# Optimization experiments

Hardware: AMD Instinct MI355X
Metric: run time of the kernel (lower is better)

Reference implementation:

```python
import jax
import jax.numpy as jnp
import numpy as np

EPS = 1e-06


def _topk_mask(scores, k):
    # scores: (T, E); hard top-k mask along last dim
    _, idx = jax.lax.top_k(scores, k)            # (T, k)
    hard = jax.nn.one_hot(idx, scores.shape[-1]).sum(axis=-2)  # (T, E)
    return hard.astype(bool)


def setup_inputs() -> dict:
    key = jax.random.key(0)
    k1, k2, k3 = jax.random.split(key, 3)
    T, D, E = 8192, 4096, 64
    h_td = jax.random.normal(k1, (T, D), dtype=jnp.float32)
    # eqx.nn.Linear weight layout: (out_features, in_features)
    W = jax.random.normal(k2, (E, D), dtype=jnp.float32) * (1.0 / np.sqrt(D))
    bias_e = jax.random.normal(k3, (E,), dtype=jnp.float32)
    return {"h_td": h_td, "W": W, "bias_e": bias_e, "k": 8}


def reference(h_td, W, bias_e, k):
    # Linear(d_model -> E), no bias in proj; external bias_e added after
    logits_te = jnp.einsum("td,ed->te", h_td, W) + bias_e[None, :]  # (T, E)
    # Soft combine weights always from clean logits
    weight_te = jax.nn.softmax(logits_te, axis=-1)
    # Training path: Gumbel noise on the selection scores only
    gkey = jax.random.key(42)
    u = jax.random.uniform(gkey, logits_te.shape, minval=EPS, maxval=1.0 - EPS)
    g = -jnp.log(-jnp.log(u))
    sel_scores = logits_te + g
    mask_te = _topk_mask(sel_scores, k)
    return (mask_te, weight_te, logits_te)
```

## Files before the change

### kernel.cpp

```cpp
#include <hip/hip_runtime.h>
#include <stdint.h>
#include <math.h>

#define T_DIM 8192
#define D_DIM 4096
#define E_DIM 64
#define TE (T_DIM * E_DIM)
#define GAP_MARGIN 2e-3
#define ROWS 32
#define BK 256
#define NCHUNK (D_DIM / BK)
#define FIX_WAVES 16
#define FIX_COLS (D_DIM / FIX_WAVES)

typedef __attribute__((ext_vector_type(8))) short short8_t;
typedef __attribute__((ext_vector_type(4))) float f32x4;

#define BAR() do {                                            \
    asm volatile("s_waitcnt lgkmcnt(0)" ::: "memory");        \
    __builtin_amdgcn_s_barrier();                             \
    asm volatile("" ::: "memory");                            \
  } while (0)

__device__ __align__(16) short Whi_g[E_DIM * D_DIM];
__device__ __align__(16) short Wlo_g[E_DIM * D_DIM];

__device__ __forceinline__ void threefry2x32_k42(uint32_t x0, uint32_t x1,
                                                 uint32_t& o0, uint32_t& o1) {
  const uint32_t ks0 = 0u, ks1 = 42u;
  const uint32_t ks2 = 0x1BD11BDAu ^ ks0 ^ ks1;
  x0 += ks0; x1 += ks1;
#define TF_RND(r) { x0 += x1; x1 = (x1 << (r)) | (x1 >> (32 - (r))); x1 ^= x0; }
  TF_RND(13) TF_RND(15) TF_RND(26) TF_RND(6)   x0 += ks1; x1 += ks2 + 1u;
  TF_RND(17) TF_RND(29) TF_RND(16) TF_RND(24)  x0 += ks2; x1 += ks0 + 2u;
  TF_RND(13) TF_RND(15) TF_RND(26) TF_RND(6)   x0 += ks0; x1 += ks1 + 3u;
  TF_RND(17) TF_RND(29) TF_RND(16) TF_RND(24)  x0 += ks1; x1 += ks2 + 4u;
  TF_RND(13) TF_RND(15) TF_RND(26) TF_RND(6)   x0 += ks2; x1 += ks0 + 5u;
#undef TF_RND
  o0 = x0; o1 = x1;
}

__device__ __forceinline__ uint32_t jax_random_bits32(uint32_t j) {
  uint32_t o0, o1;
  threefry2x32_k42(0u, j, o0, o1);
  return o0 ^ o1;
}

__device__ __forceinline__ void finalize_row_f64(double logit, int e, int t,
                                                 float& mask_out, float& weight_out,
                                                 double& gap_out) {
  double m = logit;
#pragma unroll
  for (int off = 1; off < 64; off <<= 1) {
    const double om = __shfl_xor(m, off, 64);
    m = (om > m) ? om : m;
  }
  const double pe = exp(logit - m);
  double s = pe;
#pragma unroll
  for (int off = 1; off < 64; off <<= 1) s += __shfl_xor(s, off, 64);
  weight_out = (float)(pe / s);

  const int idx = t * 64 + e;
  const uint32_t bits = jax_random_bits32((uint32_t)idx);
  const float f01 = __uint_as_float((bits >> 9) | 0x3f800000u) - 1.0f;
  const float minv = 1e-6f;
  const float maxv = 0.999999f;
  float u = __fadd_rn(__fmul_rn(f01, maxv - minv), minv);
  u = fmaxf(minv, u);
  const double g = -log(-log((double)u));
  const double sel = logit + g;

  float mask = 0.0f;
  double cur = sel;
  double v8 = 0.0, v9 = 0.0;
  for (int it = 0; it < 9; ++it) {
    double v = cur;
    int vi = e;
#pragma unroll
    for (int off = 1; off < 64; off <<= 1) {
      const double ov = __shfl_xor(v, off, 64);
      const int    oi = __shfl_xor(vi, off, 64);
      if (ov > v || (ov == v && oi < vi)) { v = ov; vi = oi; }
    }
    if (it < 8) {
      if (vi == e) { mask = 1.0f; cur = -__builtin_inf(); }
      if (it == 7) v8 = v;
    } else {
      v9 = v;
    }
  }
  mask_out = mask;
  gap_out = v8 - v9;
}

__device__ __forceinline__ uint16_t f2bf(float f) {
  const uint32_t x = __float_as_uint(f);
  return (uint16_t)((x + 0x7FFFu + ((x >> 16) & 1u)) >> 16);
}

__device__ __forceinline__ void split8(const float4 a, const float4 b,
                                       short8_t& hi, short8_t& lo) {
  const float f[8] = {a.x, a.y, a.z, a.w, b.x, b.y, b.z, b.w};
#pragma unroll
  for (int j = 0; j < 8; ++j) {
    const uint16_t hb = f2bf(f[j]);
    const float fh = __uint_as_float((uint32_t)hb << 16);
    const uint16_t lb = f2bf(f[j] - fh);
    hi[j] = (short)hb;
    lo[j] = (short)lb;
  }
}

__global__ __launch_bounds__(256)
void w_split_kernel(const float* __restrict__ W) {
  const int g = blockIdx.x * 256 + threadIdx.x;
#pragma unroll
  for (int r = 0; r < 2; ++r) {
    const int u = g * 2 + r;
    const int e = u >> 9;
    const int k0 = (u & 511) * 8;
    const float* wp = W + (size_t)e * D_DIM + k0;
    const float4 a = *reinterpret_cast<const float4*>(wp);
    const float4 b = *reinterpret_cast<const float4*>(wp + 4);
    short8_t hi, lo;
    split8(a, b, hi, lo);
    const int ks = k0 >> 5, q = (k0 >> 3) & 3;
    const int subE = e >> 4, ee = e & 15;
    const int idx = ks * 2048 + subE * 512 + q * 128 + ee * 8;
    *reinterpret_cast<short8_t*>(Whi_g + idx) = hi;
    *reinterpret_cast<short8_t*>(Wlo_g + idx) = lo;
  }
}

__global__ __launch_bounds__(512, 2)
void router_mfma_kernel(const float* __restrict__ h,
                        const float* __restrict__ bias,
                        float* __restrict__ out,
                        unsigned char* __restrict__ flags) {
  __shared__ __align__(16) short Ahi[2][ROWS * BK];
  __shared__ __align__(16) short Alo[2][ROWS * BK];
  __shared__ float logits_lds[ROWS * 65];

  const int tid  = threadIdx.x;
  const int wave = tid >> 6;
  const int lane = tid & 63;
  const int m    = wave >> 2;
  const int n    = wave & 3;
  const int row0 = blockIdx.x * ROWS;

  const int r  = tid >> 4;
  const int k0 = (tid & 15) * 16;
  const int sW  = (tid & 15) >> 1;
  const int qW  = ((tid & 15) & 1) * 2;
  const int u0A = sW * 128 + qW * 32 + r;
  const int u0B = u0A + 32;
  const int uA  = u0A ^ ((u0A >> 5) & 7);
  const int uB  = u0B ^ ((u0B >> 5) & 7);
  const float* hst = h + (size_t)(row0 + r) * D_DIM + k0;

  const int ar0 = (lane >> 4) * 32 + m * 16 + (lane & 15);

  const int b_off = n * 512 + (lane >> 4) * 128 + (lane & 15) * 8;

  f32x4 acc = {0.0f, 0.0f, 0.0f, 0.0f};

  float4 Ra0, Ra1, Ra2, Ra3, Rb0, Rb1, Rb2, Rb3;
  Ra0 = *reinterpret_cast<const float4*>(hst + 0);
  Ra1 = *reinterpret_cast<const float4*>(hst + 4);
  Ra2 = *reinterpret_cast<const float4*>(hst + 8);
  Ra3 = *reinterpret_cast<const float4*>(hst + 12);
  Rb0 = *reinterpret_cast<const float4*>(hst + BK + 0);
  Rb1 = *reinterpret_cast<const float4*>(hst + BK + 4);
  Rb2 = *reinterpret_cast<const float4*>(hst + BK + 8);
  Rb3 = *reinterpret_cast<const float4*>(hst + BK + 12);

#define KSTEP(S, BH, BL)                                                       \
  {                                                                            \
    const int ur0_ = (S) * 128 + ar0;                                          \
    const int ur_  = ur0_ ^ ((ur0_ >> 5) & 7);                                 \
    const short8_t ah_ = *reinterpret_cast<const short8_t*>(&Ahi[BUF_][ur_ * 8]); \
    const short8_t al_ = *reinterpret_cast<const short8_t*>(&Alo[BUF_][ur_ * 8]); \
    acc = __builtin_amdgcn_mfma_f32_16x16x32_bf16(al_, BH, acc, 0, 0, 0);      \
    acc = __builtin_amdgcn_mfma_f32_16x16x32_bf16(ah_, BL, acc, 0, 0, 0);      \
    acc = __builtin_amdgcn_mfma_f32_16x16x32_bf16(ah_, BH, acc, 0, 0, 0);      \
  }

#define CHUNK_STEP(R0, R1, R2, R3, BUF, CC)                                    \
  {                                                                            \
    const int BUF_ = (BUF);                                                    \
               \
    const size_t bb_ = (size_t)((CC) * 8) * 2048 + b_off;                      \
    const short8_t BH0 = *reinterpret_cast<const short8_t*>(Whi_g + bb_ + 0 * 2048); \
    const short8_t BH1 = *reinterpret_cast<const short8_t*>(Whi_g + bb_ + 1 * 2048); \
    const short8_t BH2 = *reinterpret_cast<const short8_t*>(Whi_g + bb_ + 2 * 2048); \
    const short8_t BH3 = *reinterpret_cast<const short8_t*>(Whi_g + bb_ + 3 * 2048); \
    const short8_t BH4 = *reinterpret_cast<const short8_t*>(Whi_g + bb_ + 4 * 2048); \
    const short8_t BH5 = *reinterpret_cast<const short8_t*>(Whi_g + bb_ + 5 * 2048); \
    const short8_t BH6 = *reinterpret_cast<const short8_t*>(Whi_g + bb_ + 6 * 2048); \
    const short8_t BH7 = *reinterpret_cast<const short8_t*>(Whi_g + bb_ + 7 * 2048); \
    const short8_t BL0 = *reinterpret_cast<const short8_t*>(Wlo_g + bb_ + 0 * 2048); \
    const short8_t BL1 = *reinterpret_cast<const short8_t*>(Wlo_g + bb_ + 1 * 2048); \
    const short8_t BL2 = *reinterpret_cast<const short8_t*>(Wlo_g + bb_ + 2 * 2048); \
    const short8_t BL3 = *reinterpret_cast<const short8_t*>(Wlo_g + bb_ + 3 * 2048); \
    const short8_t BL4 = *reinterpret_cast<const short8_t*>(Wlo_g + bb_ + 4 * 2048); \
    const short8_t BL5 = *reinterpret_cast<const short8_t*>(Wlo_g + bb_ + 5 * 2048); \
    const short8_t BL6 = *reinterpret_cast<const short8_t*>(Wlo_g + bb_ + 6 * 2048); \
    const short8_t BL7 = *reinterpret_cast<const short8_t*>(Wlo_g + bb_ + 7 * 2048); \
          \
    short8_t hi_, lo_;                                                         \
    split8(R0, R1, hi_, lo_);                                                  \
    *reinterpret_cast<short8_t*>(&Ahi[BUF_][uA * 8]) = hi_;                    \
    *reinterpret_cast<short8_t*>(&Alo[BUF_][uA * 8]) = lo_;                    \
    split8(R2, R3, hi_, lo_);                                                  \
    *reinterpret_cast<short8_t*>(&Ahi[BUF_][uB * 8]) = hi_;                    \
    *reinterpret_cast<short8_t*>(&Alo[BUF_][uB * 8]) = lo_;                    \
    BAR();                                                                     \
                \
    if ((CC) + 2 < NCHUNK) {                                                   \
      const float* p_ = hst + ((CC) + 2) * BK;                                 \
      R0 = *reinterpret_cast<const float4*>(p_ + 0);                           \
      R1 = *reinterpret_cast<const float4*>(p_ + 4);                           \
      R2 = *reinterpret_cast<const float4*>(p_ + 8);                           \
      R3 = *reinterpret_cast<const float4*>(p_ + 12);                          \
    }                                                                          \
    KSTEP(0, BH0, BL0) KSTEP(1, BH1, BL1) KSTEP(2, BH2, BL2)                   \
    KSTEP(3, BH3, BL3) KSTEP(4, BH4, BL4) KSTEP(5, BH5, BL5)                   \
    KSTEP(6, BH6, BL6) KSTEP(7, BH7, BL7)                                      \
  }

  for (int c = 0; c < NCHUNK; c += 2) {
    CHUNK_STEP(Ra0, Ra1, Ra2, Ra3, 0, c)
    CHUNK_STEP(Rb0, Rb1, Rb2, Rb3, 1, c + 1)
  }
#undef CHUNK_STEP
#undef KSTEP

  {
    const int q   = lane >> 4;
    const int col = n * 16 + (lane & 15);
#pragma unroll
    for (int reg = 0; reg < 4; ++reg) {
      const int mr = m * 16 + q * 4 + reg;
      logits_lds[mr * 65 + col] = acc[reg];
    }
  }
  __syncthreads();

  const int e = lane;
  const double be = (double)bias[e];
  for (int rr = 0; rr < 4; ++rr) {
    const int rloc = wave * 4 + rr;
    const int t = row0 + rloc;
    const double logit = (double)logits_lds[rloc * 65 + e] + be;

    float mask, weight;
    double gap;
    finalize_row_f64(logit, e, t, mask, weight, gap);

    const int idx = t * 64 + e;
    out[idx]          = mask;
    out[TE + idx]     = weight;
    out[2 * TE + idx] = (float)logit;
    if (e == 0) flags[t] = (gap < GAP_MARGIN) ? 1 : 0;
  }
}

__global__ __launch_bounds__(1024)
void router_fixup_kernel(const float* __restrict__ h,
                         const float* __restrict__ W,
                         const float* __restrict__ bias,
                         const unsigned char* __restrict__ flags,
                         float* __restrict__ out) {
  const int t = blockIdx.x;
  if (flags[t] == 0) return;

  __shared__ float  h_lds[D_DIM];
  __shared__ double red[FIX_WAVES][64];

  const int tid  = threadIdx.x;
  const int wv   = tid >> 6;
  const int lane = tid & 63;

  {
    const float4* hrow4 = reinterpret_cast<const float4*>(h + (size_t)t * D_DIM);
    reinterpret_cast<float4*>(h_lds)[tid] = hrow4[tid];
  }
  __syncthreads();

  const int e = lane;
  const float* wrow = W + (size_t)e * D_DIM + wv * FIX_COLS;
  const float* hseg = h_lds + wv * FIX_COLS;

  double acc0 = 0.0, acc1 = 0.0, acc2 = 0.0, acc3 = 0.0;
#pragma unroll 4
  for (int c = 0; c < FIX_COLS; c += 16) {
    const float4 w0 = *reinterpret_cast<const float4*>(wrow + c);
    const float4 w1 = *reinterpret_cast<const float4*>(wrow + c + 4);
    const float4 w2 = *reinterpret_cast<const float4*>(wrow + c + 8);
    const float4 w3 = *reinterpret_cast<const float4*>(wrow + c + 12);
    acc0 = fma((double)w0.x, (double)hseg[c + 0], acc0);
    acc0 = fma((double)w0.y, (double)hseg[c + 1], acc0);
    acc0 = fma((double)w0.z, (double)hseg[c + 2], acc0);
    acc0 = fma((double)w0.w, (double)hseg[c + 3], acc0);
    acc1 = fma((double)w1.x, (double)hseg[c + 4], acc1);
    acc1 = fma((double)w1.y, (double)hseg[c + 5], acc1);
    acc1 = fma((double)w1.z, (double)hseg[c + 6], acc1);
    acc1 = fma((double)w1.w, (double)hseg[c + 7], acc1);
    acc2 = fma((double)w2.x, (double)hseg[c + 8], acc2);
    acc2 = fma((double)w2.y, (double)hseg[c + 9], acc2);
    acc2 = fma((double)w2.z, (double)hseg[c + 10], acc2);
    acc2 = fma((double)w2.w, (double)hseg[c + 11], acc2);
    acc3 = fma((double)w3.x, (double)hseg[c + 12], acc3);
    acc3 = fma((double)w3.y, (double)hseg[c + 13], acc3);
    acc3 = fma((double)w3.z, (double)hseg[c + 14], acc3);
    acc3 = fma((double)w3.w, (double)hseg[c + 15], acc3);
  }
  red[wv][e] = (acc0 + acc1) + (acc2 + acc3);
  __syncthreads();

  if (wv == 0) {
    double s = red[0][e];
#pragma unroll
    for (int i = 1; i < FIX_WAVES; ++i) s += red[i][e];
    const double logit = s + (double)bias[e];

    float mask, weight;
    double gap;
    finalize_row_f64(logit, e, t, mask, weight, gap);

    const int idx = t * 64 + e;
    out[idx]          = mask;
    out[TE + idx]     = weight;
    out[2 * TE + idx] = (float)logit;
  }
}

extern "C" void kernel_launch(void* const* d_in, const int* in_sizes, int n_in,
                              void* d_out, int out_size, void* d_ws, size_t ws_size,
                              hipStream_t stream) {
  const float* h    = (const float*)d_in[0];
  const float* W    = (const float*)d_in[1];
  const float* bias = (const float*)d_in[2];
  float* out = (float*)d_out;
  unsigned char* flags = (unsigned char*)d_ws;

  w_split_kernel<<<64, 256, 0, stream>>>(W);
  router_mfma_kernel<<<T_DIM / ROWS, 512, 0, stream>>>(h, bias, out, flags);
  router_fixup_kernel<<<T_DIM, 1024, 0, stream>>>(h, W, bias, flags, out);
}
```

Baseline: 305.7 us.

## Restructure MFMA router to 4 waves with 2 M-tiles each, rework fixup reduction

The main kernel moves from 8 waves (2x4 M/N tiling) to 4 waves that each compute two 16-row M tiles. Each wave loads its W fragments from global once and reuses them for both tiles, halving redundant B loads per block. The h staging becomes coalesced float4 loads with a simpler, unswizzled LDS layout, and a second barrier is added per chunk. The fixup kernel now uses 512 threads, with each wave computing 8 experts over the full row via coalesced W reads and a shuffle reduction instead of per-column strided reads. Risks include LDS bank conflicts from dropping the swizzle, lower occupancy from launch_bounds(256,1), and the extra barrier.

```diff
diff --git a/kernel.cpp b/kernel.cpp
--- a/kernel.cpp
+++ b/kernel.cpp
@@ -10,8 +10,6 @@
 #define ROWS 32
 #define BK 256
 #define NCHUNK (D_DIM / BK)
-#define FIX_WAVES 16
-#define FIX_COLS (D_DIM / FIX_WAVES)
 
 typedef __attribute__((ext_vector_type(8))) short short8_t;
 typedef __attribute__((ext_vector_type(4))) float f32x4;
@@ -97,6 +95,14 @@
 __device__ __forceinline__ uint16_t f2bf(float f) {
   const uint32_t x = __float_as_uint(f);
   return (uint16_t)((x + 0x7FFFu + ((x >> 16) & 1u)) >> 16);
+}
+
+__device__ __forceinline__ void split4(const float4 v, ushort4& hi, ushort4& lo) {
+  float fh;
+  hi.x = f2bf(v.x); fh = __uint_as_float((uint32_t)hi.x << 16); lo.x = f2bf(v.x - fh);
+  hi.y = f2bf(v.y); fh = __uint_as_float((uint32_t)hi.y << 16); lo.y = f2bf(v.y - fh);
+  hi.z = f2bf(v.z); fh = __uint_as_float((uint32_t)hi.z << 16); lo.z = f2bf(v.z - fh);
+  hi.w = f2bf(v.w); fh = __uint_as_float((uint32_t)hi.w << 16); lo.w = f2bf(v.w - fh);
 }
 
 __device__ __forceinline__ void split8(const float4 a, const float4 b,
@@ -133,7 +139,7 @@
   }
 }
 
-__global__ __launch_bounds__(512, 2)
+__global__ __launch_bounds__(256, 1)
 void router_mfma_kernel(const float* __restrict__ h,
                         const float* __restrict__ bias,
                         float* __restrict__ out,
@@ -145,51 +151,59 @@
   const int tid  = threadIdx.x;
   const int wave = tid >> 6;
   const int lane = tid & 63;
-  const int m    = wave >> 2;
-  const int n    = wave & 3;
   const int row0 = blockIdx.x * ROWS;
 
-  const int r  = tid >> 4;
-  const int k0 = (tid & 15) * 16;
-  const int sW  = (tid & 15) >> 1;
-  const int qW  = ((tid & 15) & 1) * 2;
-  const int u0A = sW * 128 + qW * 32 + r;
-  const int u0B = u0A + 32;
-  const int uA  = u0A ^ ((u0A >> 5) & 7);
-  const int uB  = u0B ^ ((u0B >> 5) & 7);
-  const float* hst = h + (size_t)(row0 + r) * D_DIM + k0;
-
-  const int ar0 = (lane >> 4) * 32 + m * 16 + (lane & 15);
-
-  const int b_off = n * 512 + (lane >> 4) * 128 + (lane & 15) * 8;
-
-  f32x4 acc = {0.0f, 0.0f, 0.0f, 0.0f};
-
-  float4 Ra0, Ra1, Ra2, Ra3, Rb0, Rb1, Rb2, Rb3;
-  Ra0 = *reinterpret_cast<const float4*>(hst + 0);
-  Ra1 = *reinterpret_cast<const float4*>(hst + 4);
-  Ra2 = *reinterpret_cast<const float4*>(hst + 8);
-  Ra3 = *reinterpret_cast<const float4*>(hst + 12);
-  Rb0 = *reinterpret_cast<const float4*>(hst + BK + 0);
-  Rb1 = *reinterpret_cast<const float4*>(hst + BK + 4);
-  Rb2 = *reinterpret_cast<const float4*>(hst + BK + 8);
-  Rb3 = *reinterpret_cast<const float4*>(hst + BK + 12);
+  const int r = tid >> 3;
+  const int j = tid & 7;
+  const int qW = j >> 1, halfW = j & 1;
+  const float* hst = h + (size_t)(row0 + r) * D_DIM + j * 4;
+  const int wbase = (qW * 32 + r) * 8 + halfW * 4;
+
+  const int arbase = (lane >> 4) * 32 + (lane & 15);
+
+  const int b_off = wave * 512 + (lane >> 4) * 128 + (lane & 15) * 8;
+
+  f32x4 accA = {0.0f, 0.0f, 0.0f, 0.0f};
+  f32x4 accB = {0.0f, 0.0f, 0.0f, 0.0f};
+
+  float4 Ra0, Ra1, Ra2, Ra3, Ra4, Ra5, Ra6, Ra7;
+  float4 Rb0, Rb1, Rb2, Rb3, Rb4, Rb5, Rb6, Rb7;
+#define LOADSET(P0,P1,P2,P3,P4,P5,P6,P7, CC)                                   \
+  { const float* p_ = hst + (CC) * BK;                                         \
+    P0 = *reinterpret_cast<const float4*>(p_ + 0 * 32);                        \
+    P1 = *reinterpret_cast<const float4*>(p_ + 1 * 32);                        \
+    P2 = *reinterpret_cast<const float4*>(p_ + 2 * 32);                        \
+    P3 = *reinterpret_cast<const float4*>(p_ + 3 * 32);                        \
+    P4 = *reinterpret_cast<const float4*>(p_ + 4 * 32);                        \
+    P5 = *reinterpret_cast<const float4*>(p_ + 5 * 32);                        \
+    P6 = *reinterpret_cast<const float4*>(p_ + 6 * 32);                        \
+    P7 = *reinterpret_cast<const float4*>(p_ + 7 * 32); }
+
+  LOADSET(Ra0,Ra1,Ra2,Ra3,Ra4,Ra5,Ra6,Ra7, 0)
+  LOADSET(Rb0,Rb1,Rb2,Rb3,Rb4,Rb5,Rb6,Rb7, 1)
+
+#define SPLITW(S, RV)                                                          \
+  { ushort4 hi_, lo_;                                                          \
+    split4(RV, hi_, lo_);                                                      \
+    *reinterpret_cast<ushort4*>(&Ahi[BUF_][(S) * 1024 + wbase]) = hi_;         \
+    *reinterpret_cast<ushort4*>(&Alo[BUF_][(S) * 1024 + wbase]) = lo_; }
 
 #define KSTEP(S, BH, BL)                                                       \
-  {                                                                            \
-    const int ur0_ = (S) * 128 + ar0;                                          \
-    const int ur_  = ur0_ ^ ((ur0_ >> 5) & 7);                                 \
-    const short8_t ah_ = *reinterpret_cast<const short8_t*>(&Ahi[BUF_][ur_ * 8]); \
-    const short8_t al_ = *reinterpret_cast<const short8_t*>(&Alo[BUF_][ur_ * 8]); \
-    acc = __builtin_amdgcn_mfma_f32_16x16x32_bf16(al_, BH, acc, 0, 0, 0);      \
-    acc = __builtin_amdgcn_mfma_f32_16x16x32_bf16(ah_, BL, acc, 0, 0, 0);      \
-    acc = __builtin_amdgcn_mfma_f32_16x16x32_bf16(ah_, BH, acc, 0, 0, 0);      \
-  }
-
-#define CHUNK_STEP(R0, R1, R2, R3, BUF, CC)                                    \
-  {                                                                            \
-    const int BUF_ = (BUF);                                                    \
-               \
+  { const int u0_ = (S) * 128 + arbase;                                        \
+    const short8_t ah0 = *reinterpret_cast<const short8_t*>(&Ahi[BUF_][u0_ * 8]);        \
+    const short8_t al0 = *reinterpret_cast<const short8_t*>(&Alo[BUF_][u0_ * 8]);        \
+    const short8_t ah1 = *reinterpret_cast<const short8_t*>(&Ahi[BUF_][(u0_ + 16) * 8]); \
+    const short8_t al1 = *reinterpret_cast<const short8_t*>(&Alo[BUF_][(u0_ + 16) * 8]); \
+    accA = __builtin_amdgcn_mfma_f32_16x16x32_bf16(al0, BH, accA, 0, 0, 0);    \
+    accA = __builtin_amdgcn_mfma_f32_16x16x32_bf16(ah0, BL, accA, 0, 0, 0);    \
+    accA = __builtin_amdgcn_mfma_f32_16x16x32_bf16(ah0, BH, accA, 0, 0, 0);    \
+    accB = __builtin_amdgcn_mfma_f32_16x16x32_bf16(al1, BH, accB, 0, 0, 0);    \
+    accB = __builtin_amdgcn_mfma_f32_16x16x32_bf16(ah1, BL, accB, 0, 0, 0);    \
+    accB = __builtin_amdgcn_mfma_f32_16x16x32_bf16(ah1, BH, accB, 0, 0, 0); }
+
+#define CHUNK_STEP(P0,P1,P2,P3,P4,P5,P6,P7, BUF, CC)                           \
+  { const int BUF_ = (BUF);                                                    \
+                   \
     const size_t bb_ = (size_t)((CC) * 8) * 2048 + b_off;                      \
     const short8_t BH0 = *reinterpret_cast<const short8_t*>(Whi_g + bb_ + 0 * 2048); \
     const short8_t BH1 = *reinterpret_cast<const short8_t*>(Whi_g + bb_ + 1 * 2048); \
@@ -207,50 +221,44 @@
     const short8_t BL5 = *reinterpret_cast<const short8_t*>(Wlo_g + bb_ + 5 * 2048); \
     const short8_t BL6 = *reinterpret_cast<const short8_t*>(Wlo_g + bb_ + 6 * 2048); \
     const short8_t BL7 = *reinterpret_cast<const short8_t*>(Wlo_g + bb_ + 7 * 2048); \
-          \
-    short8_t hi_, lo_;                                                         \
-    split8(R0, R1, hi_, lo_);                                                  \
-    *reinterpret_cast<short8_t*>(&Ahi[BUF_][uA * 8]) = hi_;                    \
-    *reinterpret_cast<short8_t*>(&Alo[BUF_][uA * 8]) = lo_;                    \
-    split8(R2, R3, hi_, lo_);                                                  \
-    *reinterpret_cast<short8_t*>(&Ahi[BUF_][uB * 8]) = hi_;                    \
-    *reinterpret_cast<short8_t*>(&Alo[BUF_][uB * 8]) = lo_;                    \
+               \
+    SPLITW(0, P0) SPLITW(1, P1) SPLITW(2, P2) SPLITW(3, P3)                    \
+    SPLITW(4, P4) SPLITW(5, P5) SPLITW(6, P6) SPLITW(7, P7)                    \
     BAR();                                                                     \
                 \
     if ((CC) + 2 < NCHUNK) {                                                   \
-      const float* p_ = hst + ((CC) + 2) * BK;                                 \
-      R0 = *reinterpret_cast<const float4*>(p_ + 0);                           \
-      R1 = *reinterpret_cast<const float4*>(p_ + 4);                           \
-      R2 = *reinterpret_cast<const float4*>(p_ + 8);                           \
-      R3 = *reinterpret_cast<const float4*>(p_ + 12);                          \
+      LOADSET(P0,P1,P2,P3,P4,P5,P6,P7, (CC) + 2)                               \
     }                                                                          \
     KSTEP(0, BH0, BL0) KSTEP(1, BH1, BL1) KSTEP(2, BH2, BL2)                   \
     KSTEP(3, BH3, BL3) KSTEP(4, BH4, BL4) KSTEP(5, BH5, BL5)                   \
     KSTEP(6, BH6, BL6) KSTEP(7, BH7, BL7)                                      \
+    BAR();           \
   }
 
   for (int c = 0; c < NCHUNK; c += 2) {
-    CHUNK_STEP(Ra0, Ra1, Ra2, Ra3, 0, c)
-    CHUNK_STEP(Rb0, Rb1, Rb2, Rb3, 1, c + 1)
+    CHUNK_STEP(Ra0,Ra1,Ra2,Ra3,Ra4,Ra5,Ra6,Ra7, 0, c)
+    CHUNK_STEP(Rb0,Rb1,Rb2,Rb3,Rb4,Rb5,Rb6,Rb7, 1, c + 1)
   }
 #undef CHUNK_STEP
 #undef KSTEP
+#undef SPLITW
+#undef LOADSET
 
   {
     const int q   = lane >> 4;
-    const int col = n * 16 + (lane & 15);
+    const int col = wave * 16 + (lane & 15);
 #pragma unroll
     for (int reg = 0; reg < 4; ++reg) {
-      const int mr = m * 16 + q * 4 + reg;
-      logits_lds[mr * 65 + col] = acc[reg];
+      logits_lds[(q * 4 + reg) * 65 + col]      = accA[reg];
+      logits_lds[(16 + q * 4 + reg) * 65 + col] = accB[reg];
     }
   }
   __syncthreads();
 
   const int e = lane;
   const double be = (double)bias[e];
-  for (int rr = 0; rr < 4; ++rr) {
-    const int rloc = wave * 4 + rr;
+  for (int rr = 0; rr < 8; ++rr) {
+    const int rloc = wave * 8 + rr;
     const int t = row0 + rloc;
     const double logit = (double)logits_lds[rloc * 65 + e] + be;
 
@@ -266,7 +274,7 @@
   }
 }
 
-__global__ __launch_bounds__(1024)
+__global__ __launch_bounds__(512)
 void router_fixup_kernel(const float* __restrict__ h,
                          const float* __restrict__ W,
                          const float* __restrict__ bias,
@@ -276,7 +284,7 @@
   if (flags[t] == 0) return;
 
   __shared__ float  h_lds[D_DIM];
-  __shared__ double red[FIX_WAVES][64];
+  __shared__ double red[64];
 
   const int tid  = threadIdx.x;
   const int wv   = tid >> 6;
@@ -284,47 +292,36 @@
 
   {
     const float4* hrow4 = reinterpret_cast<const float4*>(h + (size_t)t * D_DIM);
-    reinterpret_cast<float4*>(h_lds)[tid] = hrow4[tid];
+    float4* hl4 = reinterpret_cast<float4*>(h_lds);
+    hl4[tid]       = hrow4[tid];
+    hl4[tid + 512] = hrow4[tid + 512];
   }
   __syncthreads();
 
-  const int e = lane;
-  const float* wrow = W + (size_t)e * D_DIM + wv * FIX_COLS;
-  const float* hseg = h_lds + wv * FIX_COLS;
-
-  double acc0 = 0.0, acc1 = 0.0, acc2 = 0.0, acc3 = 0.0;
-#pragma unroll 4
-  for (int c = 0; c < FIX_COLS; c += 16) {
-    const float4 w0 = *reinterpret_cast<const float4*>(wrow + c);
-    const float4 w1 = *reinterpret_cast<const float4*>(wrow + c + 4);
-    const float4 w2 = *reinterpret_cast<const float4*>(wrow + c + 8);
-    const float4 w3 = *reinterpret_cast<const float4*>(wrow + c + 12);
-    acc0 = fma((double)w0.x, (double)hseg[c + 0], acc0);
-    acc0 = fma((double)w0.y, (double)hseg[c + 1], acc0);
-    acc0 = fma((double)w0.z, (double)hseg[c + 2], acc0);
-    acc0 = fma((double)w0.w, (double)hseg[c + 3], acc0);
-    acc1 = fma((double)w1.x, (double)hseg[c + 4], acc1);
-    acc1 = fma((double)w1.y, (double)hseg[c + 5], acc1);
-    acc1 = fma((double)w1.z, (double)hseg[c + 6], acc1);
-    acc1 = fma((double)w1.w, (double)hseg[c + 7], acc1);
-    acc2 = fma((double)w2.x, (double)hseg[c + 8], acc2);
-    acc2 = fma((double)w2.y, (double)hseg[c + 9], acc2);
-    acc2 = fma((double)w2.z, (double)hseg[c + 10], acc2);
-    acc2 = fma((double)w2.w, (double)hseg[c + 11], acc2);
-    acc3 = fma((double)w3.x, (double)hseg[c + 12], acc3);
-    acc3 = fma((double)w3.y, (double)hseg[c + 13], acc3);
-    acc3 = fma((double)w3.z, (double)hseg[c + 14], acc3);
-    acc3 = fma((double)w3.w, (double)hseg[c + 15], acc3);
-  }
-  red[wv][e] = (acc0 + acc1) + (acc2 + acc3);
+  for (int ei = 0; ei < 8; ++ei) {
+    const int e = wv * 8 + ei;
+    const float4* wrow = reinterpret_cast<const float4*>(W + (size_t)e * D_DIM);
+    const float4* hl4  = reinterpret_cast<const float4*>(h_lds);
+    double a0 = 0.0, a1 = 0.0, a2 = 0.0, a3 = 0.0;
+#pragma unroll
+    for (int i = 0; i < 16; ++i) {
+      const float4 w  = wrow[i * 64 + lane];
+      const float4 hh = hl4[i * 64 + lane];
+      a0 = fma((double)w.x, (double)hh.x, a0);
+      a1 = fma((double)w.y, (double)hh.y, a1);
+      a2 = fma((double)w.z, (double)hh.z, a2);
+      a3 = fma((double)w.w, (double)hh.w, a3);
+    }
+    double s = (a0 + a1) + (a2 + a3);
+#pragma unroll
+    for (int off = 1; off < 64; off <<= 1) s += __shfl_xor(s, off, 64);
+    if (lane == 0) red[e] = s;
+  }
   __syncthreads();
 
   if (wv == 0) {
-    double s = red[0][e];
-#pragma unroll
-    for (int i = 1; i < FIX_WAVES; ++i) s += red[i][e];
-    const double logit = s + (double)bias[e];
-
+    const int e = lane;
+    const double logit = red[e] + (double)bias[e];
     float mask, weight;
     double gap;
     finalize_row_f64(logit, e, t, mask, weight, gap);
@@ -346,6 +343,6 @@
   unsigned char* flags = (unsigned char*)d_ws;
 
   w_split_kernel<<<64, 256, 0, stream>>>(W);
-  router_mfma_kernel<<<T_DIM / ROWS, 512, 0, stream>>>(h, bias, out, flags);
-  router_fixup_kernel<<<T_DIM, 1024, 0, stream>>>(h, W, bias, flags, out);
-}
+  router_mfma_kernel<<<T_DIM / ROWS, 256, 0, stream>>>(h, bias, out, flags);
+  router_fixup_kernel<<<T_DIM, 512, 0, stream>>>(h, W, bias, flags, out);
+}
```

Measured after the change: 317.6 us. 3.9% more time.
